# Kernel tuning notes

Measured on AMD Instinct MI355X. Metric: run time of the kernel, lower is better.

## Reference

```python
import jax, jax.numpy as jnp
import numpy as np

D_MODEL = 1024
NUM_HEADS = 16
D_K = D_MODEL // NUM_HEADS
ROPE_THETA = 10000.0


def setup_inputs() -> dict:
    key = jax.random.key(0)
    kx, kq, kk, kv, ko = jax.random.split(key, 5)
    B, S = 2, 2048
    sigma = np.sqrt(2.0) / np.sqrt(D_MODEL + D_MODEL)
    x = jax.random.normal(kx, (B, S, D_MODEL), dtype=jnp.float32)
    Wq = jax.random.normal(kq, (D_MODEL, D_MODEL), dtype=jnp.float32) * sigma
    Wk = jax.random.normal(kk, (D_MODEL, D_MODEL), dtype=jnp.float32) * sigma
    Wv = jax.random.normal(kv, (D_MODEL, D_MODEL), dtype=jnp.float32) * sigma
    Wo = jax.random.normal(ko, (D_MODEL, D_MODEL), dtype=jnp.float32) * sigma
    return {"x": x, "Wq": Wq, "Wk": Wk, "Wv": Wv, "Wo": Wo}


def _rope(t, positions):
    # t: [B, H, S, D_K], positions: [S]
    half = jnp.arange(0, D_K, 2, dtype=jnp.float32)          # [D_K/2]
    freqs = 1.0 / (ROPE_THETA ** (half / D_K))               # [D_K/2]
    angles = positions[:, None].astype(jnp.float32) * freqs  # [S, D_K/2]
    cos = jnp.cos(angles)
    sin = jnp.sin(angles)
    t_even = t[..., 0::2]
    t_odd = t[..., 1::2]
    even_rot = t_even * cos - t_odd * sin
    odd_rot = t_even * sin + t_odd * cos
    # interleave back to [..., D_K]
    return jnp.stack([even_rot, odd_rot], axis=-1).reshape(t.shape)


def reference(x, Wq, Wk, Wv, Wo):
    B, S, _ = x.shape
    # weight layout is [d_out, d_in]: y = x @ W.T
    def proj(W):
        y = jnp.einsum('bsd,ed->bse', x, W)
        return y.reshape(B, S, NUM_HEADS, D_K).transpose(0, 2, 1, 3)  # [B,H,S,Dk]
    Q, K, V = proj(Wq), proj(Wk), proj(Wv)
    positions = jnp.arange(S)
    Q = _rope(Q, positions)
    K = _rope(K, positions)
    scale = 1.0 / jnp.sqrt(jnp.asarray(D_K, dtype=x.dtype))
    scores = jnp.einsum('bhqd,bhkd->bhqk', Q, K) * scale  # [B,H,S,S]
    causal = jnp.tril(jnp.ones((S, S), dtype=bool))
    scores = jnp.where(causal, scores, -jnp.inf)
    probs = jax.nn.softmax(scores, axis=-1)
    out = jnp.einsum('bhqk,bhkd->bhqd', probs, V)          # [B,H,S,Dk]
    out = out.transpose(0, 2, 1, 3).reshape(B, S, D_MODEL)
    return jnp.einsum('bsd,ed->bse', out, Wo)
```

## Files before the change

### kernel.cpp

```cpp
#include <hip/hip_runtime.h>
#include <hip/hip_bf16.h>
#include <math.h>

#define S_LEN   2048
#define BATCH   2
#define DMODEL  1024
#define NHEADS  16
#define DKH     64
#define MROWS   (BATCH * S_LEN)

typedef __attribute__((ext_vector_type(8))) __bf16 bf16x8;
typedef __attribute__((ext_vector_type(4))) float f32x4;
typedef __attribute__((ext_vector_type(8))) unsigned short u16x8;

__device__ __forceinline__ float bfu2f(unsigned short u) {
    union { unsigned int i; float f; } v;
    v.i = ((unsigned int)u) << 16;
    return v.f;
}

__device__ __forceinline__ unsigned short f2bfu(float f) {
    union { __bf16 h; unsigned short u; } v;
    v.h = (__bf16)f;
    return v.u;
}

#define LGKM0() __builtin_amdgcn_s_waitcnt(0xc07f)

#define SROW 40

__global__ __launch_bounds__(256) void cvt_w(
    const float* __restrict__ W0, const float* __restrict__ W1, const float* __restrict__ W2,
    unsigned short* __restrict__ Wb)
{
    const float* W = (blockIdx.y == 0) ? W0 : (blockIdx.y == 1) ? W1 : W2;
    size_t idx = ((size_t)blockIdx.x * 256 + threadIdx.x) * 8;
    float4 a = *(const float4*)(W + idx);
    float4 b = *(const float4*)(W + idx + 4);
    u16x8 h;
    h[0] = f2bfu(a.x); h[1] = f2bfu(a.y); h[2] = f2bfu(a.z); h[3] = f2bfu(a.w);
    h[4] = f2bfu(b.x); h[5] = f2bfu(b.y); h[6] = f2bfu(b.z); h[7] = f2bfu(b.w);
    *(u16x8*)(Wb + (size_t)blockIdx.y * (DMODEL * DMODEL) + idx) = h;
}

__global__ __launch_bounds__(256) void gemm_qkv(
    const float* __restrict__ X,
    const unsigned short* __restrict__ Wb,
    unsigned short* __restrict__ Yq, unsigned short* __restrict__ Yk, unsigned short* __restrict__ Yv)
{
    __shared__ __align__(16) unsigned char pool[36864];
    unsigned short* As = (unsigned short*)pool;
    unsigned short* Bs = As + 128 * SROW;

    const int tid  = threadIdx.x;
    const int wave = tid >> 6;
    const int lane = tid & 63;
    const int c    = lane & 15;
    const int quad = lane >> 4;

    const int m0 = blockIdx.y * 128;
    const int n0 = blockIdx.x * 128;
    const int w_idx = n0 >> 10;
    const int e0    = n0 & 1023;
    const unsigned short* Wsrc = Wb + (size_t)w_idx * (DMODEL * DMODEL);

    const int mhalf = (wave & 1) * 64;
    const int nhalf = (wave >> 1) * 64;

    f32x4 acc[4][4];
#pragma unroll
    for (int i = 0; i < 4; i++)
#pragma unroll
        for (int j = 0; j < 4; j++) acc[i][j] = (f32x4){0.f, 0.f, 0.f, 0.f};

    const int lrow = tid >> 3;
    const int lkq  = tid & 7;
    const int brow = tid >> 2;
    const int bchk = (tid & 3) * 8;

    for (int k0 = 0; k0 < DMODEL; k0 += 32) {
        __syncthreads();
#pragma unroll
        for (int i = 0; i < 4; i++) {
            int row = i * 32 + lrow;
            float4 v = *(const float4*)(X + (size_t)(m0 + row) * DMODEL + k0 + lkq * 4);
            ushort4 h;
            h.x = f2bfu(v.x); h.y = f2bfu(v.y); h.z = f2bfu(v.z); h.w = f2bfu(v.w);
            *(ushort4*)(&As[row * SROW + lkq * 4]) = h;
        }
#pragma unroll
        for (int i = 0; i < 2; i++) {
            int row = i * 64 + brow;
            *(u16x8*)(&Bs[row * SROW + bchk]) =
                *(const u16x8*)(Wsrc + (size_t)(e0 + row) * DMODEL + k0 + bchk);
        }
        __syncthreads();

        bf16x8 af[4], bfr[4];
#pragma unroll
        for (int mt = 0; mt < 4; mt++)
            af[mt] = *(const bf16x8*)(&As[(mhalf + mt * 16 + c) * SROW + quad * 8]);
#pragma unroll
        for (int nt = 0; nt < 4; nt++)
            bfr[nt] = *(const bf16x8*)(&Bs[(nhalf + nt * 16 + c) * SROW + quad * 8]);
#pragma unroll
        for (int mt = 0; mt < 4; mt++)
#pragma unroll
            for (int nt = 0; nt < 4; nt++)
                acc[mt][nt] = __builtin_amdgcn_mfma_f32_16x16x32_bf16(af[mt], bfr[nt], acc[mt][nt], 0, 0, 0);
    }

    __syncthreads();

    const int h = (e0 + nhalf) >> 6;
    if (w_idx < 2) {
        unsigned short* Yqk = (w_idx == 0) ? Yq : Yk;
        float* EPf = (float*)pool + wave * 16 * 68;
        const int row = lane >> 2;
        const int cg  = lane & 3;
#pragma unroll
        for (int mt = 0; mt < 4; mt++) {
            LGKM0();
#pragma unroll
            for (int nt = 0; nt < 4; nt++)
#pragma unroll
                for (int r = 0; r < 4; r++)
                    EPf[(quad * 4 + r) * 68 + nt * 16 + c] = acc[mt][nt][r];
            LGKM0();
            float fl[16];
#pragma unroll
            for (int j = 0; j < 4; j++) {
                float4 v = *(const float4*)(&EPf[row * 68 + cg * 16 + j * 4]);
                fl[j * 4 + 0] = v.x; fl[j * 4 + 1] = v.y;
                fl[j * 4 + 2] = v.z; fl[j * 4 + 3] = v.w;
            }
            int m = m0 + mhalf + mt * 16 + row;
            int s = m & (S_LEN - 1);
            int b = m >> 11;
            u16x8 o0, o1;
#pragma unroll
            for (int pi = 0; pi < 8; pi++) {
                int p = cg * 8 + pi;
                float freq  = exp2f(-(float)p * 0.41524101186092034f);
                float angle = (float)s * freq;
                float sn, cs;
                __sincosf(angle, &sn, &cs);
                float ev = fl[2 * pi], ov = fl[2 * pi + 1];
                float re = ev * cs - ov * sn;
                float ro = ev * sn + ov * cs;
                if (pi < 4) { o0[2 * pi] = f2bfu(re); o0[2 * pi + 1] = f2bfu(ro); }
                else        { o1[2 * (pi - 4)] = f2bfu(re); o1[2 * (pi - 4) + 1] = f2bfu(ro); }
            }
            unsigned short* dst = Yqk + (((size_t)(b * NHEADS + h)) * S_LEN + s) * DKH + cg * 16;
            *(u16x8*)(dst)     = o0;
            *(u16x8*)(dst + 8) = o1;
        }
    } else {
        unsigned short* EPb = (unsigned short*)pool + wave * 64 * 72;
        LGKM0();
#pragma unroll
        for (int nt = 0; nt < 4; nt++)
#pragma unroll
            for (int mt = 0; mt < 4; mt++)
#pragma unroll
                for (int r = 0; r < 4; r++)
                    EPb[(nt * 16 + c) * 72 + mt * 16 + quad * 4 + r] = f2bfu(acc[mt][nt][r]);
        LGKM0();
        int mbase = m0 + mhalf;
        int s0 = mbase & (S_LEN - 1);
        int b  = mbase >> 11;
        unsigned short* dst = Yv + (((size_t)(b * NHEADS + h)) * DKH + lane) * S_LEN + s0;
#pragma unroll
        for (int j = 0; j < 8; j++)
            *(u16x8*)(dst + j * 8) = *(const u16x8*)(&EPb[lane * 72 + j * 8]);
    }
}

__global__ __launch_bounds__(256) void gemm_wo(
    const unsigned short* __restrict__ X,
    const float* __restrict__ W,
    float* __restrict__ Yf)
{
    __shared__ __align__(16) unsigned char pool[27648];
    unsigned short* As = (unsigned short*)pool;
    unsigned short* Bs = As + 64 * 72;

    const int tid  = threadIdx.x;
    const int wave = tid >> 6;
    const int lane = tid & 63;
    const int c    = lane & 15;
    const int quad = lane >> 4;

    const int m0 = blockIdx.y * 64;
    const int n0 = blockIdx.x * 128;

    const int mhalf = (wave & 1) * 32;
    const int nhalf = (wave >> 1) * 64;

    f32x4 acc[2][4];
#pragma unroll
    for (int i = 0; i < 2; i++)
#pragma unroll
        for (int j = 0; j < 4; j++) acc[i][j] = (f32x4){0.f, 0.f, 0.f, 0.f};

    const int srow = tid >> 3;
    const int scol = (tid & 7) * 8;

    for (int k0 = 0; k0 < DMODEL; k0 += 64) {
        __syncthreads();
#pragma unroll
        for (int i = 0; i < 2; i++) {
            int row = i * 32 + srow;
            *(u16x8*)(&As[row * 72 + scol]) =
                *(const u16x8*)(X + (size_t)(m0 + row) * DMODEL + k0 + scol);
        }
#pragma unroll
        for (int i = 0; i < 4; i++) {
            int row = i * 32 + srow;
            const float* p = W + (size_t)(n0 + row) * DMODEL + k0 + scol;
            float4 va = *(const float4*)(p);
            float4 vb = *(const float4*)(p + 4);
            u16x8 h;
            h[0] = f2bfu(va.x); h[1] = f2bfu(va.y); h[2] = f2bfu(va.z); h[3] = f2bfu(va.w);
            h[4] = f2bfu(vb.x); h[5] = f2bfu(vb.y); h[6] = f2bfu(vb.z); h[7] = f2bfu(vb.w);
            *(u16x8*)(&Bs[row * 72 + scol]) = h;
        }
        __syncthreads();

#pragma unroll
        for (int half = 0; half < 2; half++) {
            bf16x8 af[2], bfr[4];
#pragma unroll
            for (int mt = 0; mt < 2; mt++)
                af[mt] = *(const bf16x8*)(&As[(mhalf + mt * 16 + c) * 72 + half * 32 + quad * 8]);
#pragma unroll
            for (int nt = 0; nt < 4; nt++)
                bfr[nt] = *(const bf16x8*)(&Bs[(nhalf + nt * 16 + c) * 72 + half * 32 + quad * 8]);
#pragma unroll
            for (int mt = 0; mt < 2; mt++)
#pragma unroll
                for (int nt = 0; nt < 4; nt++)
                    acc[mt][nt] = __builtin_amdgcn_mfma_f32_16x16x32_bf16(af[mt], bfr[nt], acc[mt][nt], 0, 0, 0);
        }
    }

    __syncthreads();

    float* EPf = (float*)pool + wave * 16 * 68;
    const int row = lane >> 2;
    const int cg  = lane & 3;
#pragma unroll
    for (int mt = 0; mt < 2; mt++) {
        LGKM0();
#pragma unroll
        for (int nt = 0; nt < 4; nt++)
#pragma unroll
            for (int r = 0; r < 4; r++)
                EPf[(quad * 4 + r) * 68 + nt * 16 + c] = acc[mt][nt][r];
        LGKM0();
        int m = m0 + mhalf + mt * 16 + row;
        float* dst = Yf + (size_t)m * DMODEL + n0 + nhalf + cg * 16;
#pragma unroll
        for (int j = 0; j < 4; j++)
            *(float4*)(dst + j * 4) = *(const float4*)(&EPf[row * 68 + cg * 16 + j * 4]);
    }
}

__global__ __launch_bounds__(256, 4) void attn_mfma(
    const unsigned short* __restrict__ Q,
    const unsigned short* __restrict__ K,
    const unsigned short* __restrict__ Vt,
    unsigned short* __restrict__ A)
{
    __shared__ unsigned short Ks[32 * 72];
    __shared__ unsigned short Vs[64 * 40];
    __shared__ unsigned short Plds[4][16 * 40];

    const int tid  = threadIdx.x;
    const int wave = tid >> 6;
    const int lane = tid & 63;
    const int c    = lane & 15;
    const int quad = lane >> 4;

    const int bh = blockIdx.x;
    const int b  = bh >> 4;
    const int h  = bh & 15;
    const int qb = (int)(gridDim.y - 1) - (int)blockIdx.y;
    const int q0b = qb * 64;
    const int q0 = q0b + wave * 16;

    const unsigned short* Qb = Q  + (size_t)bh * S_LEN * DKH;
    const unsigned short* Kb = K  + (size_t)bh * S_LEN * DKH;
    const unsigned short* Vb = Vt + (size_t)bh * DKH * S_LEN;

    bf16x8 qf0 = *(const bf16x8*)(Qb + (q0 + c) * DKH + quad * 8);
    bf16x8 qf1 = *(const bf16x8*)(Qb + (q0 + c) * DKH + 32 + quad * 8);

    f32x4 o0 = {0.f,0.f,0.f,0.f}, o1 = o0, o2 = o0, o3 = o0;
    float l[4] = {0.f, 0.f, 0.f, 0.f};

    unsigned short* Pw = &Plds[wave][0];

    const int my_nkb   = (q0 + 16 + 31) >> 5;
    const int nkb_blk  = (q0b + 64 + 31) >> 5;
    const int kb_full  = (q0 >= 31) ? (((q0 - 31) >> 5) + 1) : 0;

    const int krow  = tid >> 3;
    const int kcol8 = (tid & 7) * 8;
    const int vrow  = tid >> 2;
    const int vcol8 = (tid & 3) * 8;

    uint4 gK = *(const uint4*)(Kb + (size_t)krow * DKH + kcol8);
    uint4 gV = *(const uint4*)(Vb + (size_t)vrow * S_LEN + vcol8);

    for (int kb = 0; kb < nkb_blk; kb++) {
        const int k0 = kb * 32;
        __syncthreads();
        *(uint4*)(&Ks[krow * 72 + kcol8]) = gK;
        *(uint4*)(&Vs[vrow * 40 + vcol8]) = gV;
        __syncthreads();
        if (kb + 1 < nkb_blk) {
            gK = *(const uint4*)(Kb + (size_t)(k0 + 32 + krow) * DKH + kcol8);
            gV = *(const uint4*)(Vb + (size_t)vrow * S_LEN + k0 + 32 + vcol8);
        }
        if (kb < my_nkb) {
            bf16x8 k00 = *(const bf16x8*)(&Ks[c * 72 + quad * 8]);
            bf16x8 k01 = *(const bf16x8*)(&Ks[c * 72 + 32 + quad * 8]);
            bf16x8 k10 = *(const bf16x8*)(&Ks[(16 + c) * 72 + quad * 8]);
            bf16x8 k11 = *(const bf16x8*)(&Ks[(16 + c) * 72 + 32 + quad * 8]);
            f32x4 s0 = {0.f,0.f,0.f,0.f}, s1 = {0.f,0.f,0.f,0.f};
            s0 = __builtin_amdgcn_mfma_f32_16x16x32_bf16(qf0, k00, s0, 0, 0, 0);
            s0 = __builtin_amdgcn_mfma_f32_16x16x32_bf16(qf1, k01, s0, 0, 0, 0);
            s1 = __builtin_amdgcn_mfma_f32_16x16x32_bf16(qf0, k10, s1, 0, 0, 0);
            s1 = __builtin_amdgcn_mfma_f32_16x16x32_bf16(qf1, k11, s1, 0, 0, 0);

            if (kb < kb_full) {
#pragma unroll
                for (int r = 0; r < 4; r++) {
                    float e0 = __expf(s0[r] * 0.125f);
                    float e1 = __expf(s1[r] * 0.125f);
                    unsigned short pb0 = f2bfu(e0);
                    unsigned short pb1 = f2bfu(e1);
                    Pw[(quad * 4 + r) * 40 + c]      = pb0;
                    Pw[(quad * 4 + r) * 40 + 16 + c] = pb1;
                    l[r] += bfu2f(pb0) + bfu2f(pb1);
                }
            } else {
#pragma unroll
                for (int r = 0; r < 4; r++) {
                    int qrow = q0 + quad * 4 + r;
                    float e0 = (k0 + c      <= qrow) ? __expf(s0[r] * 0.125f) : 0.0f;
                    float e1 = (k0 + 16 + c <= qrow) ? __expf(s1[r] * 0.125f) : 0.0f;
                    unsigned short pb0 = f2bfu(e0);
                    unsigned short pb1 = f2bfu(e1);
                    Pw[(quad * 4 + r) * 40 + c]      = pb0;
                    Pw[(quad * 4 + r) * 40 + 16 + c] = pb1;
                    l[r] += bfu2f(pb0) + bfu2f(pb1);
                }
            }
            LGKM0();

            bf16x8 pf = *(const bf16x8*)(Pw + c * 40 + quad * 8);

            bf16x8 vf0 = *(const bf16x8*)(&Vs[(0 * 16 + c) * 40 + quad * 8]);
            bf16x8 vf1 = *(const bf16x8*)(&Vs[(1 * 16 + c) * 40 + quad * 8]);
            bf16x8 vf2 = *(const bf16x8*)(&Vs[(2 * 16 + c) * 40 + quad * 8]);
            bf16x8 vf3 = *(const bf16x8*)(&Vs[(3 * 16 + c) * 40 + quad * 8]);
            o0 = __builtin_amdgcn_mfma_f32_16x16x32_bf16(pf, vf0, o0, 0, 0, 0);
            o1 = __builtin_amdgcn_mfma_f32_16x16x32_bf16(pf, vf1, o1, 0, 0, 0);
            o2 = __builtin_amdgcn_mfma_f32_16x16x32_bf16(pf, vf2, o2, 0, 0, 0);
            o3 = __builtin_amdgcn_mfma_f32_16x16x32_bf16(pf, vf3, o3, 0, 0, 0);
        }
    }

#pragma unroll
    for (int m = 1; m < 16; m <<= 1) {
#pragma unroll
        for (int r = 0; r < 4; r++) l[r] += __shfl_xor(l[r], m, 64);
    }

#pragma unroll
    for (int r = 0; r < 4; r++) {
        float inv = 1.0f / l[r];
        int s = q0 + quad * 4 + r;
        unsigned short* Ap = A + ((size_t)b * S_LEN + s) * DMODEL + h * DKH;
        Ap[0 * 16 + c] = f2bfu(o0[r] * inv);
        Ap[1 * 16 + c] = f2bfu(o1[r] * inv);
        Ap[2 * 16 + c] = f2bfu(o2[r] * inv);
        Ap[3 * 16 + c] = f2bfu(o3[r] * inv);
    }
}

extern "C" void kernel_launch(void* const* d_in, const int* in_sizes, int n_in,
                              void* d_out, int out_size, void* d_ws, size_t ws_size,
                              hipStream_t stream) {
    const float* x  = (const float*)d_in[0];
    const float* Wq = (const float*)d_in[1];
    const float* Wk = (const float*)d_in[2];
    const float* Wv = (const float*)d_in[3];
    const float* Wo = (const float*)d_in[4];
    float* out = (float*)d_out;

    unsigned short* Qw = (unsigned short*)d_ws;
    unsigned short* Kw = Qw + (size_t)MROWS * DMODEL;
    unsigned short* Vw = Kw + (size_t)MROWS * DMODEL;
    unsigned short* Wb = Vw + (size_t)MROWS * DMODEL;
    unsigned short* Aw = Wb;

    cvt_w<<<dim3(DMODEL * DMODEL / (256 * 8), 3), 256, 0, stream>>>(Wq, Wk, Wv, Wb);

    gemm_qkv<<<dim3(3 * DMODEL / 128, MROWS / 128), 256, 0, stream>>>(
        x, Wb, Qw, Kw, Vw);

    attn_mfma<<<dim3(NHEADS * BATCH, S_LEN / 64), 256, 0, stream>>>(Qw, Kw, Vw, Aw);

    gemm_wo<<<dim3(DMODEL / 128, MROWS / 64), 256, 0, stream>>>(Aw, Wo, out);
}
```

Baseline: 196.0 us.

## Pre-convert X and Wo to bf16 and stage GEMM tiles via global_load_lds

```diff
diff --git a/kernel.cpp b/kernel.cpp
--- a/kernel.cpp
+++ b/kernel.cpp
@@ -27,30 +27,57 @@
 
 #define LGKM0() __builtin_amdgcn_s_waitcnt(0xc07f)
 
-#define SROW 40
-
-__global__ __launch_bounds__(256) void cvt_w(
+__device__ __forceinline__ void gload_lds16(const void* g, void* l) {
+    __builtin_amdgcn_global_load_lds(
+        (const __attribute__((address_space(1))) void*)g,
+        (__attribute__((address_space(3))) void*)l, 16, 0, 0);
+}
+
+__global__ __launch_bounds__(256) void cvt_all(
     const float* __restrict__ W0, const float* __restrict__ W1, const float* __restrict__ W2,
-    unsigned short* __restrict__ Wb)
+    const float* __restrict__ X,
+    unsigned short* __restrict__ Wb,
+    unsigned short* __restrict__ Xb)
 {
-    const float* W = (blockIdx.y == 0) ? W0 : (blockIdx.y == 1) ? W1 : W2;
+    const int y = blockIdx.y;
+    const float* src;
+    unsigned short* dst;
+    if (y < 3) {
+        src = (y == 0) ? W0 : (y == 1) ? W1 : W2;
+        dst = Wb + (size_t)y * (DMODEL * DMODEL);
+    } else {
+        src = X + (size_t)(y - 3) * (DMODEL * DMODEL);
+        dst = Xb + (size_t)(y - 3) * (DMODEL * DMODEL);
+    }
+    size_t idx = ((size_t)blockIdx.x * 256 + threadIdx.x) * 8;
+    float4 a = *(const float4*)(src + idx);
+    float4 b = *(const float4*)(src + idx + 4);
+    u16x8 h;
+    h[0] = f2bfu(a.x); h[1] = f2bfu(a.y); h[2] = f2bfu(a.z); h[3] = f2bfu(a.w);
+    h[4] = f2bfu(b.x); h[5] = f2bfu(b.y); h[6] = f2bfu(b.z); h[7] = f2bfu(b.w);
+    *(u16x8*)(dst + idx) = h;
+}
+
+__global__ __launch_bounds__(256) void cvt_wo(
+    const float* __restrict__ W, unsigned short* __restrict__ Wob)
+{
     size_t idx = ((size_t)blockIdx.x * 256 + threadIdx.x) * 8;
     float4 a = *(const float4*)(W + idx);
     float4 b = *(const float4*)(W + idx + 4);
     u16x8 h;
     h[0] = f2bfu(a.x); h[1] = f2bfu(a.y); h[2] = f2bfu(a.z); h[3] = f2bfu(a.w);
     h[4] = f2bfu(b.x); h[5] = f2bfu(b.y); h[6] = f2bfu(b.z); h[7] = f2bfu(b.w);
-    *(u16x8*)(Wb + (size_t)blockIdx.y * (DMODEL * DMODEL) + idx) = h;
+    *(u16x8*)(Wob + idx) = h;
 }
 
 __global__ __launch_bounds__(256) void gemm_qkv(
-    const float* __restrict__ X,
+    const unsigned short* __restrict__ Xb,
     const unsigned short* __restrict__ Wb,
     unsigned short* __restrict__ Yq, unsigned short* __restrict__ Yk, unsigned short* __restrict__ Yv)
 {
     __shared__ __align__(16) unsigned char pool[36864];
     unsigned short* As = (unsigned short*)pool;
-    unsigned short* Bs = As + 128 * SROW;
+    unsigned short* Bs = As + 128 * 32;
 
     const int tid  = threadIdx.x;
     const int wave = tid >> 6;
@@ -73,36 +100,29 @@
 #pragma unroll
         for (int j = 0; j < 4; j++) acc[i][j] = (f32x4){0.f, 0.f, 0.f, 0.f};
 
-    const int lrow = tid >> 3;
-    const int lkq  = tid & 7;
-    const int brow = tid >> 2;
-    const int bchk = (tid & 3) * 8;
+    const int srow = wave * 32 + (lane >> 2);
+    const int scol = (lane & 3) * 8;
+    const unsigned short* Asrc = Xb   + (size_t)(m0 + srow) * DMODEL + scol;
+    const unsigned short* Bsrc = Wsrc + (size_t)(e0 + srow) * DMODEL + scol;
+    unsigned short* Adst = As + srow * 32 + scol;
+    unsigned short* Bdst = Bs + srow * 32 + scol;
 
     for (int k0 = 0; k0 < DMODEL; k0 += 32) {
         __syncthreads();
 #pragma unroll
-        for (int i = 0; i < 4; i++) {
-            int row = i * 32 + lrow;
-            float4 v = *(const float4*)(X + (size_t)(m0 + row) * DMODEL + k0 + lkq * 4);
-            ushort4 h;
-            h.x = f2bfu(v.x); h.y = f2bfu(v.y); h.z = f2bfu(v.z); h.w = f2bfu(v.w);
-            *(ushort4*)(&As[row * SROW + lkq * 4]) = h;
+        for (int j = 0; j < 2; j++) {
+            gload_lds16(Asrc + (size_t)(j * 16) * DMODEL + k0, Adst + j * 16 * 32);
+            gload_lds16(Bsrc + (size_t)(j * 16) * DMODEL + k0, Bdst + j * 16 * 32);
         }
-#pragma unroll
-        for (int i = 0; i < 2; i++) {
-            int row = i * 64 + brow;
-            *(u16x8*)(&Bs[row * SROW + bchk]) =
-                *(const u16x8*)(Wsrc + (size_t)(e0 + row) * DMODEL + k0 + bchk);
-        }
         __syncthreads();
 
         bf16x8 af[4], bfr[4];
 #pragma unroll
         for (int mt = 0; mt < 4; mt++)
-            af[mt] = *(const bf16x8*)(&As[(mhalf + mt * 16 + c) * SROW + quad * 8]);
+            af[mt] = *(const bf16x8*)(&As[(mhalf + mt * 16 + c) * 32 + quad * 8]);
 #pragma unroll
         for (int nt = 0; nt < 4; nt++)
-            bfr[nt] = *(const bf16x8*)(&Bs[(nhalf + nt * 16 + c) * SROW + quad * 8]);
+            bfr[nt] = *(const bf16x8*)(&Bs[(nhalf + nt * 16 + c) * 32 + quad * 8]);
 #pragma unroll
         for (int mt = 0; mt < 4; mt++)
 #pragma unroll
@@ -178,12 +198,12 @@
 
 __global__ __launch_bounds__(256) void gemm_wo(
     const unsigned short* __restrict__ X,
-    const float* __restrict__ W,
+    const unsigned short* __restrict__ Wob,
     float* __restrict__ Yf)
 {
-    __shared__ __align__(16) unsigned char pool[27648];
+    __shared__ __align__(16) unsigned char pool[18432];
     unsigned short* As = (unsigned short*)pool;
-    unsigned short* Bs = As + 64 * 72;
+    unsigned short* Bs = As + 64 * 32;
 
     const int tid  = threadIdx.x;
     const int wave = tid >> 6;
@@ -203,45 +223,34 @@
 #pragma unroll
         for (int j = 0; j < 4; j++) acc[i][j] = (f32x4){0.f, 0.f, 0.f, 0.f};
 
-    const int srow = tid >> 3;
-    const int scol = (tid & 7) * 8;
-
-    for (int k0 = 0; k0 < DMODEL; k0 += 64) {
-        __syncthreads();
-#pragma unroll
-        for (int i = 0; i < 2; i++) {
-            int row = i * 32 + srow;
-            *(u16x8*)(&As[row * 72 + scol]) =
-                *(const u16x8*)(X + (size_t)(m0 + row) * DMODEL + k0 + scol);
-        }
-#pragma unroll
-        for (int i = 0; i < 4; i++) {
-            int row = i * 32 + srow;
-            const float* p = W + (size_t)(n0 + row) * DMODEL + k0 + scol;
-            float4 va = *(const float4*)(p);
-            float4 vb = *(const float4*)(p + 4);
-            u16x8 h;
-            h[0] = f2bfu(va.x); h[1] = f2bfu(va.y); h[2] = f2bfu(va.z); h[3] = f2bfu(va.w);
-            h[4] = f2bfu(vb.x); h[5] = f2bfu(vb.y); h[6] = f2bfu(vb.z); h[7] = f2bfu(vb.w);
-            *(u16x8*)(&Bs[row * 72 + scol]) = h;
-        }
-        __syncthreads();
-
-#pragma unroll
-        for (int half = 0; half < 2; half++) {
-            bf16x8 af[2], bfr[4];
-#pragma unroll
-            for (int mt = 0; mt < 2; mt++)
-                af[mt] = *(const bf16x8*)(&As[(mhalf + mt * 16 + c) * 72 + half * 32 + quad * 8]);
+    const int arow = wave * 16 + (lane >> 2);
+    const int brow = wave * 32 + (lane >> 2);
+    const int scol = (lane & 3) * 8;
+    const unsigned short* Asrc = X   + (size_t)(m0 + arow) * DMODEL + scol;
+    const unsigned short* Bsrc = Wob + (size_t)(n0 + brow) * DMODEL + scol;
+    unsigned short* Adst = As + arow * 32 + scol;
+    unsigned short* Bdst = Bs + brow * 32 + scol;
+
+    for (int k0 = 0; k0 < DMODEL; k0 += 32) {
+        __syncthreads();
+        gload_lds16(Asrc + k0, Adst);
+#pragma unroll
+        for (int j = 0; j < 2; j++)
+            gload_lds16(Bsrc + (size_t)(j * 16) * DMODEL + k0, Bdst + j * 16 * 32);
+        __syncthreads();
+
+        bf16x8 af[2], bfr[4];
+#pragma unroll
+        for (int mt = 0; mt < 2; mt++)
+            af[mt] = *(const bf16x8*)(&As[(mhalf + mt * 16 + c) * 32 + quad * 8]);
+#pragma unroll
+        for (int nt = 0; nt < 4; nt++)
+            bfr[nt] = *(const bf16x8*)(&Bs[(nhalf + nt * 16 + c) * 32 + quad * 8]);
+#pragma unroll
+        for (int mt = 0; mt < 2; mt++)
 #pragma unroll
             for (int nt = 0; nt < 4; nt++)
-                bfr[nt] = *(const bf16x8*)(&Bs[(nhalf + nt * 16 + c) * 72 + half * 32 + quad * 8]);
-#pragma unroll
-            for (int mt = 0; mt < 2; mt++)
-#pragma unroll
-                for (int nt = 0; nt < 4; nt++)
-                    acc[mt][nt] = __builtin_amdgcn_mfma_f32_16x16x32_bf16(af[mt], bfr[nt], acc[mt][nt], 0, 0, 0);
-        }
+                acc[mt][nt] = __builtin_amdgcn_mfma_f32_16x16x32_bf16(af[mt], bfr[nt], acc[mt][nt], 0, 0, 0);
     }
 
     __syncthreads();
@@ -406,13 +415,17 @@
     unsigned short* Vw = Kw + (size_t)MROWS * DMODEL;
     unsigned short* Wb = Vw + (size_t)MROWS * DMODEL;
     unsigned short* Aw = Wb;
-
-    cvt_w<<<dim3(DMODEL * DMODEL / (256 * 8), 3), 256, 0, stream>>>(Wq, Wk, Wv, Wb);
+    unsigned short* Wob = Qw;
+    unsigned short* Xb = (unsigned short*)d_out;
+
+    cvt_all<<<dim3(DMODEL * DMODEL / (256 * 8), 7), 256, 0, stream>>>(Wq, Wk, Wv, x, Wb, Xb);
 
     gemm_qkv<<<dim3(3 * DMODEL / 128, MROWS / 128), 256, 0, stream>>>(
-        x, Wb, Qw, Kw, Vw);
+        Xb, Wb, Qw, Kw, Vw);
 
     attn_mfma<<<dim3(NHEADS * BATCH, S_LEN / 64), 256, 0, stream>>>(Qw, Kw, Vw, Aw);
 
-    gemm_wo<<<dim3(DMODEL / 128, MROWS / 64), 256, 0, stream>>>(Aw, Wo, out);
-}
+    cvt_wo<<<dim3(DMODEL * DMODEL / (256 * 8)), 256, 0, stream>>>(Wo, Wob);
+
+    gemm_wo<<<dim3(DMODEL / 128, MROWS / 64), 256, 0, stream>>>(Aw, Wob, out);
+}
```

Measured after the change: 207.0 us. +5.6%, slower.
